# Performance work log

Measured on AMD Instinct MI355X. Metric: run time of the kernel, lower is better.

The kernel has to match this reference:

```python
import jax, jax.numpy as jnp
import numpy as np

B, C, T = 32, 256, 4096


def _depthwise(x, w, pad):
    # x: [B, C, T], w: [C, 1, k] (torch grouped-conv layout), groups = C
    return jax.lax.conv_general_dilated(
        x, w, window_strides=(1,), padding=[(pad, pad)],
        dimension_numbers=("NCH", "OIH", "NCH"), feature_group_count=x.shape[1])


def setup_inputs() -> dict:
    key = jax.random.key(0)
    ks = jax.random.split(key, 9)
    def u(k, shape, fan_in):
        s = 1.0 / np.sqrt(fan_in)
        return jax.random.uniform(k, shape, jnp.float32, -s, s)
    return {
        "x": jax.random.normal(ks[0], (B, C, T), jnp.float32),
        "w1": u(ks[1], (C, C, 1), C),      # 1x1 conv, full depth
        "b1": u(ks[2], (C,), C),
        "w3": u(ks[3], (C, 1, 3), 3),      # 1x3 depthwise (groups=C)
        "b3": u(ks[4], (C,), 3),
        "w5": u(ks[5], (C, 1, 5), 5),      # 1x5 depthwise (groups=C)
        "b5": u(ks[6], (C,), 5),
        "wc": u(ks[7], (C, 3, 1), 3),      # combine: Conv1d(3C, C, 1, groups=C)
        "bc": u(ks[8], (C,), 3),
    }


def reference(x, w1, b1, w3, b3, w5, b5, wc, bc):
    a = jax.nn.gelu(x, approximate=False)  # torch GELU default is exact erf
    # 1x1 conv over all channels == per-timestep GEMM
    out1 = jnp.einsum("bct,oc->bot", a, w1[:, :, 0]) + b1[None, :, None]
    out3 = _depthwise(a, w3, 1) + b3[None, :, None]
    out5 = _depthwise(a, w5, 2) + b5[None, :, None]
    # per-channel interleave: [c0_1, c0_3, c0_5, c1_1, ...] -> [B, C, 3, T]
    inter = jnp.stack((out1, out3, out5), axis=2)
    # grouped 1x1 combine conv (groups=C): each output channel mixes its 3 branch outputs
    out = jnp.einsum("bcjt,cj->bct", inter, wc[:, :, 0]) + bc[None, :, None]
    return out + x
```

## Files before the change

kernel.cpp:

```cpp
#include <hip/hip_runtime.h>
#include <stdint.h>

#define BATCH 32
#define CH    256
#define TLEN  4096
#define TN    32
#define NT    8
#define NRW   36
#define TPAD  4100
#define SST   36

typedef short    bf16x8 __attribute__((ext_vector_type(8)));
typedef float    f32x4  __attribute__((ext_vector_type(4)));
typedef uint16_t u16x4  __attribute__((ext_vector_type(4)));
typedef uint16_t u16x8  __attribute__((ext_vector_type(8)));

__device__ __attribute__((aligned(16))) uint16_t g_wpk[CH * CH];
__device__ __attribute__((aligned(16))) float g_tap[5 * CH];
__device__ __attribute__((aligned(16))) float g_bias[CH];

static __device__ __forceinline__ uint16_t f32_to_bf16(float f) {
    uint32_t u = __builtin_bit_cast(uint32_t, f);
    u += 0x7FFFu + ((u >> 16) & 1u);
    return (uint16_t)(u >> 16);
}
static __device__ __forceinline__ float bf16_to_f32(uint16_t h) {
    uint32_t u = ((uint32_t)h) << 16;
    return __builtin_bit_cast(float, u);
}
static __device__ __forceinline__ float gelu_fast(float x) {
    const float A = 2.3022082f;
    const float B = 0.10294331f;
    float x2 = x * x;
    float z  = x * fmaf(x2, B, A);
    float e  = exp2f(z);
    float r  = __builtin_amdgcn_rcpf(1.0f + e);
    return fmaf(-x, r, x);
}

__global__ void prep_kernel(const float* __restrict__ w1, const float* __restrict__ b1,
                            const float* __restrict__ w3, const float* __restrict__ b3,
                            const float* __restrict__ w5, const float* __restrict__ b5,
                            const float* __restrict__ wc, const float* __restrict__ bc) {
    const int o = blockIdx.x;
    const int c = threadIdx.x;
    const float wc0 = wc[o * 3 + 0];
    const int s = c >> 5, g = (c >> 3) & 3, e = c & 7;
    g_wpk[(s * CH + o) * 32 + g * 8 + e] = f32_to_bf16(wc0 * w1[o * CH + c]);
    if (c == 0) {
        const float wc1 = wc[o * 3 + 1], wc2 = wc[o * 3 + 2];
        g_tap[0 * CH + o] = wc2 * w5[o * 5 + 0];
        g_tap[1 * CH + o] = wc1 * w3[o * 3 + 0] + wc2 * w5[o * 5 + 1];
        g_tap[2 * CH + o] = wc1 * w3[o * 3 + 1] + wc2 * w5[o * 5 + 2];
        g_tap[3 * CH + o] = wc1 * w3[o * 3 + 2] + wc2 * w5[o * 5 + 3];
        g_tap[4 * CH + o] = wc2 * w5[o * 5 + 4];
        g_bias[o] = wc0 * b1[o] + wc1 * b3[o] + wc2 * b5[o] + bc[o];
    }
}

__global__ __launch_bounds__(256, 4)
void gelu_tr_kernel(const float* __restrict__ x, uint16_t* __restrict__ aT) {
    __shared__ __attribute__((aligned(16))) uint16_t sL[64 * 72];

    const int tid = threadIdx.x;
    const int tb = blockIdx.x, cb = blockIdx.y, b = blockIdx.z;
    const int t0 = tb * 64, c0 = cb * 64;

    {
        const int cr = tid >> 2;
        const int q  = tid & 3;
        const float* xr = x + ((size_t)(b * CH + c0 + cr)) * TLEN + t0 + q * 16;
        f32x4 v0 = *(const f32x4*)(xr + 0);
        f32x4 v1 = *(const f32x4*)(xr + 4);
        f32x4 v2 = *(const f32x4*)(xr + 8);
        f32x4 v3 = *(const f32x4*)(xr + 12);
        u16x8 p0, p1;
#pragma unroll
        for (int j = 0; j < 4; ++j) {
            p0[j]     = f32_to_bf16(gelu_fast(v0[j]));
            p0[4 + j] = f32_to_bf16(gelu_fast(v1[j]));
            p1[j]     = f32_to_bf16(gelu_fast(v2[j]));
            p1[4 + j] = f32_to_bf16(gelu_fast(v3[j]));
        }
        const int b0 = (((q * 2 + 0) ^ (cr >> 3)) << 3);
        const int b1 = (((q * 2 + 1) ^ (cr >> 3)) << 3);
        *(u16x8*)(&sL[cr * 72 + b0]) = p0;
        *(u16x8*)(&sL[cr * 72 + b1]) = p1;
    }
    __syncthreads();

    uint16_t* aTb = aT + (size_t)b * TPAD * CH;
#pragma unroll
    for (int i = 0; i < 2; ++i) {
        const int idx = tid + i * 256;
        const int tr  = idx >> 3;
        const int ch  = idx & 7;
        const int t   = t0 + tr;
        const int swz = (t & 7) << 3;
        const int cin = (tr & 7) | ((((tr >> 3) ^ ch) & 7) << 3);
        u16x8 o;
#pragma unroll
        for (int j = 0; j < 8; ++j) o[j] = sL[(ch * 8 + j) * 72 + cin];
        *(u16x8*)(&aTb[(size_t)(2 + t) * CH + ((c0 + ch * 8) ^ swz)]) = o;
    }
    if (tb == 0) {
        const int pr = tid >> 6;
        const int cc = c0 + (tid & 63);
        const int prow = (pr < 2) ? pr : (4098 + (pr - 2));
        const int tmod = (pr < 2) ? (6 + pr) : (pr - 2);
        aTb[(size_t)prow * CH + (cc ^ (tmod << 3))] = 0;
    }
}

__global__ __launch_bounds__(512, 2)
void gemm_kernel(const uint16_t* __restrict__ aT, const float* __restrict__ x,
                 float* __restrict__ out) {
    __shared__ __attribute__((aligned(16))) uint16_t sA[2][NRW * CH];

    const int tid  = threadIdx.x;
    const int lane = tid & 63;
    const int wid  = tid >> 6;
    const int b    = blockIdx.y;
    const int t0b  = blockIdx.x * (TN * NT);

    const float* __restrict__ xb = x + (size_t)b * CH * TLEN;
    float* __restrict__ ob = out + (size_t)b * CH * TLEN;
    const u16x8* __restrict__ gB = (const u16x8*)(aT + (size_t)b * TPAD * CH);

    const int m0   = wid * 32;
    const int colt = lane & 15;
    const int kgrp = (lane >> 4) * 8;
    const int rg   = (lane >> 4) * 4;
    const int ci   = lane >> 2;
    const int q4   = lane & 3;
    const bool tail = (tid < 128);

    bf16x8 wfr[8][2];
#pragma unroll
    for (int s = 0; s < 8; ++s)
#pragma unroll
        for (int mi = 0; mi < 2; ++mi) {
            const int co = m0 + mi * 16 + colt;
            wfr[s][mi] = *(const bf16x8*)(g_wpk + (s * CH + co) * 32 + kgrp);
        }

    {
        const u16x8* g0 = gB + (size_t)t0b * 32;
        u16x8 s0_ = g0[tid];
        u16x8 s1_ = g0[tid + 512];
        u16x8 sT_;
        if (tail) sT_ = g0[tid + 1024];
        u16x8* d = (u16x8*)sA[0];
        d[tid] = s0_; d[tid + 512] = s1_;
        if (tail) d[tid + 1024] = sT_;
    }
    __syncthreads();

    const int swzB = (colt & 7) << 3;
    int rowB[2];
#pragma unroll
    for (int ni = 0; ni < 2; ++ni) rowB[ni] = (ni * 16 + colt + 2) * CH;
    int swzA[5];
#pragma unroll
    for (int k = 0; k < 5; ++k) swzA[k] = ((colt + k + 6) & 7) << 3;

    for (int i = 0; i < NT; ++i) {
        const int cur = i & 1, nxt = cur ^ 1;
        const int t0 = t0b + i * TN;

        u16x8 p0, p1, pT;
        if (i + 1 < NT) {
            const u16x8* gn = gB + (size_t)(t0 + TN) * 32;
            p0 = gn[tid];
            p1 = gn[tid + 512];
            if (tail) pT = gn[tid + 1024];
        }
        f32x4 xv[2][2];
#pragma unroll
        for (int mi = 0; mi < 2; ++mi) {
            const int cc = m0 + mi * 16 + ci;
            const float* xr = xb + (size_t)cc * TLEN + t0 + q4 * 8;
            xv[mi][0] = *(const f32x4*)(xr + 0);
            xv[mi][1] = *(const f32x4*)(xr + 4);
        }

        const uint16_t* __restrict__ sAc = sA[cur];

        f32x4 acc[2][2];
        const f32x4 vzero = {0.f, 0.f, 0.f, 0.f};
#pragma unroll
        for (int mi = 0; mi < 2; ++mi)
#pragma unroll
            for (int ni = 0; ni < 2; ++ni) acc[mi][ni] = vzero;

        bf16x8 bfb[2][2];
#pragma unroll
        for (int ni = 0; ni < 2; ++ni)
            bfb[0][ni] = *(const bf16x8*)(&sAc[rowB[ni] + (kgrp ^ swzB)]);
#pragma unroll
        for (int s = 0; s < 8; ++s) {
            const int c2 = s & 1, nx = c2 ^ 1;
            if (s < 7) {
                const int cin = (s + 1) * 32 + kgrp;
#pragma unroll
                for (int ni = 0; ni < 2; ++ni)
                    bfb[nx][ni] = *(const bf16x8*)(&sAc[rowB[ni] + (cin ^ swzB)]);
            }
#pragma unroll
            for (int mi = 0; mi < 2; ++mi)
#pragma unroll
                for (int ni = 0; ni < 2; ++ni)
                    acc[mi][ni] = __builtin_amdgcn_mfma_f32_16x16x32_bf16(wfr[s][mi], bfb[c2][ni], acc[mi][ni], 0, 0, 0);
        }

#pragma unroll
        for (int mi = 0; mi < 2; ++mi) {
            const int c = m0 + mi * 16 + rg;
            const f32x4 tp0 = *(const f32x4*)(g_tap + 0 * CH + c);
            const f32x4 tp1 = *(const f32x4*)(g_tap + 1 * CH + c);
            const f32x4 tp2 = *(const f32x4*)(g_tap + 2 * CH + c);
            const f32x4 tp3 = *(const f32x4*)(g_tap + 3 * CH + c);
            const f32x4 tp4 = *(const f32x4*)(g_tap + 4 * CH + c);
            const f32x4 bsv = *(const f32x4*)(g_bias + c);
#pragma unroll
            for (int ni = 0; ni < 2; ++ni) {
                const int t = ni * 16 + colt;
                u16x4 a0 = *(const u16x4*)(&sAc[(t + 0) * CH + (c ^ swzA[0])]);
                u16x4 a1 = *(const u16x4*)(&sAc[(t + 1) * CH + (c ^ swzA[1])]);
                u16x4 a2 = *(const u16x4*)(&sAc[(t + 2) * CH + (c ^ swzA[2])]);
                u16x4 a3 = *(const u16x4*)(&sAc[(t + 3) * CH + (c ^ swzA[3])]);
                u16x4 a4 = *(const u16x4*)(&sAc[(t + 4) * CH + (c ^ swzA[4])]);
#pragma unroll
                for (int r = 0; r < 4; ++r) {
                    float d = tp0[r] * bf16_to_f32(a0[r]);
                    d = fmaf(tp1[r], bf16_to_f32(a1[r]), d);
                    d = fmaf(tp2[r], bf16_to_f32(a2[r]), d);
                    d = fmaf(tp3[r], bf16_to_f32(a3[r]), d);
                    d = fmaf(tp4[r], bf16_to_f32(a4[r]), d);
                    acc[mi][ni][r] += d + bsv[r];
                }
            }
        }
        __syncthreads();

        float* __restrict__ sw = ((float*)sA[cur]) + wid * (16 * SST);
#pragma unroll
        for (int mi = 0; mi < 2; ++mi) {
#pragma unroll
            for (int ni = 0; ni < 2; ++ni) {
                const int t = ni * 16 + colt;
#pragma unroll
                for (int r = 0; r < 4; ++r) sw[(rg + r) * SST + t] = acc[mi][ni][r];
            }
            const int cc = m0 + mi * 16 + ci;
            float* orow = ob + (size_t)cc * TLEN + t0 + q4 * 8;
            const float* srow = sw + ci * SST + q4 * 8;
            f32x4 s0 = *(const f32x4*)(srow + 0);
            f32x4 s1 = *(const f32x4*)(srow + 4);
            *(f32x4*)(orow + 0) = s0 + xv[mi][0];
            *(f32x4*)(orow + 4) = s1 + xv[mi][1];
        }

        if (i + 1 < NT) {
            u16x8* d = (u16x8*)sA[nxt];
            d[tid] = p0; d[tid + 512] = p1;
            if (tail) d[tid + 1024] = pT;
        }
        __syncthreads();
    }
}

extern "C" void kernel_launch(void* const* d_in, const int* in_sizes, int n_in,
                              void* d_out, int out_size, void* d_ws, size_t ws_size,
                              hipStream_t stream) {
    const float* x  = (const float*)d_in[0];
    const float* w1 = (const float*)d_in[1];
    const float* b1 = (const float*)d_in[2];
    const float* w3 = (const float*)d_in[3];
    const float* b3 = (const float*)d_in[4];
    const float* w5 = (const float*)d_in[5];
    const float* b5 = (const float*)d_in[6];
    const float* wc = (const float*)d_in[7];
    const float* bc = (const float*)d_in[8];
    float* out = (float*)d_out;
    uint16_t* aT = (uint16_t*)d_ws;

    prep_kernel<<<dim3(CH), dim3(CH), 0, stream>>>(w1, b1, w3, b3, w5, b5, wc, bc);
    gelu_tr_kernel<<<dim3(TLEN / 64, CH / 64, BATCH), dim3(256), 0, stream>>>(x, aT);
    gemm_kernel<<<dim3(TLEN / (TN * NT), BATCH), dim3(512), 0, stream>>>(aT, x, out);
}
```

Before: 104.5 us.

## Fuse GELU/transpose into GEMM kernel with ring-buffered shared activations

Drops the separate GELU+transpose kernel and its bf16 workspace round-trip. The GEMM kernel now reads x directly, applies GELU, and writes transposed bf16 rows into a 64-row circular shared-memory buffer, staging the next 32 timesteps during each iteration and handling the halo at the sequence edges. This removes one launch and a global write plus read of the activation tensor. In exchange, each block does GELU work inline, and its x loads are less coalesced (scalar loads for the halo, per-channel rows for staging).

```diff
diff --git a/kernel.cpp b/kernel.cpp
--- a/kernel.cpp
+++ b/kernel.cpp
@@ -6,14 +6,12 @@
 #define TLEN  4096
 #define TN    32
 #define NT    8
-#define NRW   36
-#define TPAD  4100
+#define RNG   64
 #define SST   36
 
 typedef short    bf16x8 __attribute__((ext_vector_type(8)));
 typedef float    f32x4  __attribute__((ext_vector_type(4)));
 typedef uint16_t u16x4  __attribute__((ext_vector_type(4)));
-typedef uint16_t u16x8  __attribute__((ext_vector_type(8)));
 
 __device__ __attribute__((aligned(16))) uint16_t g_wpk[CH * CH];
 __device__ __attribute__((aligned(16))) float g_tap[5 * CH];
@@ -58,74 +56,20 @@
     }
 }
 
-__global__ __launch_bounds__(256, 4)
-void gelu_tr_kernel(const float* __restrict__ x, uint16_t* __restrict__ aT) {
-    __shared__ __attribute__((aligned(16))) uint16_t sL[64 * 72];
-
-    const int tid = threadIdx.x;
-    const int tb = blockIdx.x, cb = blockIdx.y, b = blockIdx.z;
-    const int t0 = tb * 64, c0 = cb * 64;
-
-    {
-        const int cr = tid >> 2;
-        const int q  = tid & 3;
-        const float* xr = x + ((size_t)(b * CH + c0 + cr)) * TLEN + t0 + q * 16;
-        f32x4 v0 = *(const f32x4*)(xr + 0);
-        f32x4 v1 = *(const f32x4*)(xr + 4);
-        f32x4 v2 = *(const f32x4*)(xr + 8);
-        f32x4 v3 = *(const f32x4*)(xr + 12);
-        u16x8 p0, p1;
-#pragma unroll
-        for (int j = 0; j < 4; ++j) {
-            p0[j]     = f32_to_bf16(gelu_fast(v0[j]));
-            p0[4 + j] = f32_to_bf16(gelu_fast(v1[j]));
-            p1[j]     = f32_to_bf16(gelu_fast(v2[j]));
-            p1[4 + j] = f32_to_bf16(gelu_fast(v3[j]));
-        }
-        const int b0 = (((q * 2 + 0) ^ (cr >> 3)) << 3);
-        const int b1 = (((q * 2 + 1) ^ (cr >> 3)) << 3);
-        *(u16x8*)(&sL[cr * 72 + b0]) = p0;
-        *(u16x8*)(&sL[cr * 72 + b1]) = p1;
-    }
-    __syncthreads();
-
-    uint16_t* aTb = aT + (size_t)b * TPAD * CH;
-#pragma unroll
-    for (int i = 0; i < 2; ++i) {
-        const int idx = tid + i * 256;
-        const int tr  = idx >> 3;
-        const int ch  = idx & 7;
-        const int t   = t0 + tr;
-        const int swz = (t & 7) << 3;
-        const int cin = (tr & 7) | ((((tr >> 3) ^ ch) & 7) << 3);
-        u16x8 o;
-#pragma unroll
-        for (int j = 0; j < 8; ++j) o[j] = sL[(ch * 8 + j) * 72 + cin];
-        *(u16x8*)(&aTb[(size_t)(2 + t) * CH + ((c0 + ch * 8) ^ swz)]) = o;
-    }
-    if (tb == 0) {
-        const int pr = tid >> 6;
-        const int cc = c0 + (tid & 63);
-        const int prow = (pr < 2) ? pr : (4098 + (pr - 2));
-        const int tmod = (pr < 2) ? (6 + pr) : (pr - 2);
-        aTb[(size_t)prow * CH + (cc ^ (tmod << 3))] = 0;
-    }
-}
-
 __global__ __launch_bounds__(512, 2)
-void gemm_kernel(const uint16_t* __restrict__ aT, const float* __restrict__ x,
-                 float* __restrict__ out) {
-    __shared__ __attribute__((aligned(16))) uint16_t sA[2][NRW * CH];
+void fused_kernel(const float* __restrict__ x, float* __restrict__ out) {
+    __shared__ __attribute__((aligned(16))) uint16_t sR[RNG * CH];
+    __shared__ __attribute__((aligned(16))) float    sS[8 * 16 * SST];
 
     const int tid  = threadIdx.x;
     const int lane = tid & 63;
     const int wid  = tid >> 6;
     const int b    = blockIdx.y;
     const int t0b  = blockIdx.x * (TN * NT);
+    const bool lastb = (blockIdx.x == gridDim.x - 1);
 
     const float* __restrict__ xb = x + (size_t)b * CH * TLEN;
     float* __restrict__ ob = out + (size_t)b * CH * TLEN;
-    const u16x8* __restrict__ gB = (const u16x8*)(aT + (size_t)b * TPAD * CH);
 
     const int m0   = wid * 32;
     const int colt = lane & 15;
@@ -133,7 +77,8 @@
     const int rg   = (lane >> 4) * 4;
     const int ci   = lane >> 2;
     const int q4   = lane & 3;
-    const bool tail = (tid < 128);
+    const int sch  = m0 + (lane >> 1);
+    const int sth  = (lane & 1) * 16;
 
     bf16x8 wfr[8][2];
 #pragma unroll
@@ -145,46 +90,44 @@
         }
 
     {
-        const u16x8* g0 = gB + (size_t)t0b * 32;
-        u16x8 s0_ = g0[tid];
-        u16x8 s1_ = g0[tid + 512];
-        u16x8 sT_;
-        if (tail) sT_ = g0[tid + 1024];
-        u16x8* d = (u16x8*)sA[0];
-        d[tid] = s0_; d[tid + 512] = s1_;
-        if (tail) d[tid + 1024] = sT_;
+#pragma unroll
+        for (int h = 0; h < 2; ++h) {
+            const int flat = tid + h * 512;
+            const int e = flat >> 8;
+            const int c = flat & 255;
+            const int gt = t0b - 2 + e;
+            float v = 0.0f;
+            if (blockIdx.x > 0 || gt >= 0) v = xb[(size_t)c * TLEN + gt];
+            sR[e * CH + (c ^ (((e + 6) & 7) << 3))] = f32_to_bf16(gelu_fast(v));
+        }
+    }
+    {
+        const float* xr = xb + (size_t)sch * TLEN + t0b + 2 + sth;
+        f32x4 v[4];
+#pragma unroll
+        for (int j = 0; j < 4; ++j) v[j] = *(const f32x4*)(xr + j * 4);
+#pragma unroll
+        for (int j = 0; j < 16; ++j) {
+            const int rr = 4 + sth + j;
+            const int sz = ((2 + sth + j) & 7) << 3;
+            sR[rr * CH + (sch ^ sz)] = f32_to_bf16(gelu_fast(v[j >> 2][j & 3]));
+        }
     }
     __syncthreads();
 
+    int swzA[5];
+#pragma unroll
+    for (int k = 0; k < 5; ++k) swzA[k] = ((colt + k + 6) & 7) << 3;
     const int swzB = (colt & 7) << 3;
-    int rowB[2];
-#pragma unroll
-    for (int ni = 0; ni < 2; ++ni) rowB[ni] = (ni * 16 + colt + 2) * CH;
-    int swzA[5];
-#pragma unroll
-    for (int k = 0; k < 5; ++k) swzA[k] = ((colt + k + 6) & 7) << 3;
 
     for (int i = 0; i < NT; ++i) {
-        const int cur = i & 1, nxt = cur ^ 1;
-        const int t0 = t0b + i * TN;
-
-        u16x8 p0, p1, pT;
-        if (i + 1 < NT) {
-            const u16x8* gn = gB + (size_t)(t0 + TN) * 32;
-            p0 = gn[tid];
-            p1 = gn[tid + 512];
-            if (tail) pT = gn[tid + 1024];
-        }
-        f32x4 xv[2][2];
-#pragma unroll
-        for (int mi = 0; mi < 2; ++mi) {
-            const int cc = m0 + mi * 16 + ci;
-            const float* xr = xb + (size_t)cc * TLEN + t0 + q4 * 8;
-            xv[mi][0] = *(const f32x4*)(xr + 0);
-            xv[mi][1] = *(const f32x4*)(xr + 4);
-        }
-
-        const uint16_t* __restrict__ sAc = sA[cur];
+        const int base = 32 * i;
+        const int t0   = t0b + base;
+
+        int rowB[2];
+#pragma unroll
+        for (int ni = 0; ni < 2; ++ni)
+            rowB[ni] = ((base + 2 + ni * 16 + colt) & 63) * CH;
 
         f32x4 acc[2][2];
         const f32x4 vzero = {0.f, 0.f, 0.f, 0.f};
@@ -196,7 +139,7 @@
         bf16x8 bfb[2][2];
 #pragma unroll
         for (int ni = 0; ni < 2; ++ni)
-            bfb[0][ni] = *(const bf16x8*)(&sAc[rowB[ni] + (kgrp ^ swzB)]);
+            bfb[0][ni] = *(const bf16x8*)(&sR[rowB[ni] + (kgrp ^ swzB)]);
 #pragma unroll
         for (int s = 0; s < 8; ++s) {
             const int c2 = s & 1, nx = c2 ^ 1;
@@ -204,7 +147,7 @@
                 const int cin = (s + 1) * 32 + kgrp;
 #pragma unroll
                 for (int ni = 0; ni < 2; ++ni)
-                    bfb[nx][ni] = *(const bf16x8*)(&sAc[rowB[ni] + (cin ^ swzB)]);
+                    bfb[nx][ni] = *(const bf16x8*)(&sR[rowB[ni] + (cin ^ swzB)]);
             }
 #pragma unroll
             for (int mi = 0; mi < 2; ++mi)
@@ -225,11 +168,16 @@
 #pragma unroll
             for (int ni = 0; ni < 2; ++ni) {
                 const int t = ni * 16 + colt;
-                u16x4 a0 = *(const u16x4*)(&sAc[(t + 0) * CH + (c ^ swzA[0])]);
-                u16x4 a1 = *(const u16x4*)(&sAc[(t + 1) * CH + (c ^ swzA[1])]);
-                u16x4 a2 = *(const u16x4*)(&sAc[(t + 2) * CH + (c ^ swzA[2])]);
-                u16x4 a3 = *(const u16x4*)(&sAc[(t + 3) * CH + (c ^ swzA[3])]);
-                u16x4 a4 = *(const u16x4*)(&sAc[(t + 4) * CH + (c ^ swzA[4])]);
+                const int r0 = ((base + t + 0) & 63) * CH;
+                const int r1 = ((base + t + 1) & 63) * CH;
+                const int r2 = ((base + t + 2) & 63) * CH;
+                const int r3 = ((base + t + 3) & 63) * CH;
+                const int r4 = ((base + t + 4) & 63) * CH;
+                u16x4 a0 = *(const u16x4*)(&sR[r0 + (c ^ swzA[0])]);
+                u16x4 a1 = *(const u16x4*)(&sR[r1 + (c ^ swzA[1])]);
+                u16x4 a2 = *(const u16x4*)(&sR[r2 + (c ^ swzA[2])]);
+                u16x4 a3 = *(const u16x4*)(&sR[r3 + (c ^ swzA[3])]);
+                u16x4 a4 = *(const u16x4*)(&sR[r4 + (c ^ swzA[4])]);
 #pragma unroll
                 for (int r = 0; r < 4; ++r) {
                     float d = tp0[r] * bf16_to_f32(a0[r]);
@@ -243,7 +191,32 @@
         }
         __syncthreads();
 
-        float* __restrict__ sw = ((float*)sA[cur]) + wid * (16 * SST);
+        f32x4 xv[2][2];
+#pragma unroll
+        for (int mi = 0; mi < 2; ++mi) {
+            const int cc = m0 + mi * 16 + ci;
+            const float* xr = xb + (size_t)cc * TLEN + t0 + q4 * 8;
+            xv[mi][0] = *(const f32x4*)(xr + 0);
+            xv[mi][1] = *(const f32x4*)(xr + 4);
+        }
+        f32x4 sv[4];
+        const bool doStage = (i + 1 < NT);
+        if (doStage) {
+            const int tau0 = t0b + 32 * (i + 1) + 2 + sth;
+            const float* xr = xb + (size_t)sch * TLEN + tau0;
+            if (!lastb || i != 6) {
+#pragma unroll
+                for (int j = 0; j < 4; ++j) sv[j] = *(const f32x4*)(xr + j * 4);
+            } else {
+#pragma unroll
+                for (int j = 0; j < 4; ++j)
+#pragma unroll
+                    for (int e = 0; e < 4; ++e)
+                        sv[j][e] = (tau0 + j * 4 + e < TLEN) ? xr[j * 4 + e] : 0.0f;
+            }
+        }
+
+        float* __restrict__ sw = sS + wid * (16 * SST);
 #pragma unroll
         for (int mi = 0; mi < 2; ++mi) {
 #pragma unroll
@@ -261,10 +234,14 @@
             *(f32x4*)(orow + 4) = s1 + xv[mi][1];
         }
 
-        if (i + 1 < NT) {
-            u16x8* d = (u16x8*)sA[nxt];
-            d[tid] = p0; d[tid + 512] = p1;
-            if (tail) d[tid + 1024] = pT;
+        if (doStage) {
+            const int rb = (32 * (i + 1) + 4) & 63;
+#pragma unroll
+            for (int j = 0; j < 16; ++j) {
+                const int rr = (rb + sth + j) & 63;
+                const int sz = ((2 + sth + j) & 7) << 3;
+                sR[rr * CH + (sch ^ sz)] = f32_to_bf16(gelu_fast(sv[j >> 2][j & 3]));
+            }
         }
         __syncthreads();
     }
@@ -283,9 +260,7 @@
     const float* wc = (const float*)d_in[7];
     const float* bc = (const float*)d_in[8];
     float* out = (float*)d_out;
-    uint16_t* aT = (uint16_t*)d_ws;
 
     prep_kernel<<<dim3(CH), dim3(CH), 0, stream>>>(w1, b1, w3, b3, w5, b5, wc, bc);
-    gelu_tr_kernel<<<dim3(TLEN / 64, CH / 64, BATCH), dim3(256), 0, stream>>>(x, aT);
-    gemm_kernel<<<dim3(TLEN / (TN * NT), BATCH), dim3(512), 0, stream>>>(aT, x, out);
-}
+    fused_kernel<<<dim3(TLEN / (TN * NT), BATCH), dim3(512), 0, stream>>>(x, out);
+}
```

Result: slower. 120.9 us (+15.8%).
